# Optimization experiments

Measured on AMD Instinct MI355X. Metric: run time of the kernel, lower is better.

## Reference

```python
import jax, jax.numpy as jnp
import numpy as np

N_EMBD = 1024
N_HEAD = 16
LATENT = 64
HEAD_DIM = N_EMBD // N_HEAD
B, T = 2, 2048
SCALE = 1.0 / np.sqrt(LATENT)


def setup_inputs() -> dict:
    key = jax.random.key(0)
    ks = jax.random.split(key, 10)
    s = lambda fan_in: 1.0 / np.sqrt(fan_in)
    return {
        "x": jax.random.normal(ks[0], (B, T, N_EMBD), dtype=jnp.float32),
        "Wq": jax.random.normal(ks[1], (N_EMBD, N_EMBD), dtype=jnp.float32) * s(N_EMBD),
        "bq": jnp.zeros((N_EMBD,), dtype=jnp.float32),
        "Wk": jax.random.normal(ks[2], (N_EMBD, N_HEAD * LATENT), dtype=jnp.float32) * s(N_EMBD),
        "bk": jnp.zeros((N_HEAD * LATENT,), dtype=jnp.float32),
        "Wv": jax.random.normal(ks[3], (N_EMBD, N_HEAD * LATENT), dtype=jnp.float32) * s(N_EMBD),
        "bv": jnp.zeros((N_HEAD * LATENT,), dtype=jnp.float32),
        "Wo": jax.random.normal(ks[4], (N_HEAD * LATENT, N_EMBD), dtype=jnp.float32) * s(N_HEAD * LATENT),
        "bo": jnp.zeros((N_EMBD,), dtype=jnp.float32),
        "Wc": jax.random.normal(ks[5], (HEAD_DIM, LATENT), dtype=jnp.float32) * s(HEAD_DIM),
    }


def reference(x, Wq, bq, Wk, bk, Wv, bv, Wo, bo, Wc):
    Bv, Tv, C = x.shape
    # projections
    q = (x @ Wq + bq).reshape(Bv, Tv, N_HEAD, HEAD_DIM)        # [B,T,H,Dh]
    k = (x @ Wk + bk).reshape(Bv, Tv, N_HEAD, LATENT)          # [B,T,H,L]
    v = (x @ Wv + bv).reshape(Bv, Tv, N_HEAD, LATENT)          # [B,T,H,L]
    # compress q into latent dim: [B,T,H,L]
    qc = jnp.einsum("bthd,dl->bthl", q, Wc)
    # attention scores [B,H,T,T]
    att = jnp.einsum("bthl,bshl->bhts", qc, k) * SCALE
    causal = jnp.tril(jnp.ones((Tv, Tv), dtype=bool))
    att = jnp.where(causal[None, None], att, -jnp.inf)
    att = jax.nn.softmax(att, axis=-1)
    y = jnp.einsum("bhts,bshl->bthl", att, v).reshape(Bv, Tv, N_HEAD * LATENT)
    return y @ Wo + bo
```

## Files before the change

kernel.cpp:

```cpp
#include <hip/hip_runtime.h>
#include <stdint.h>

#define TT 2048
#define BB 2
#define MROWS (BB*TT)
#define LSCALE 0.18033688011112043f

typedef unsigned short u16;
typedef __bf16 bf16x8 __attribute__((ext_vector_type(8)));
typedef float f32x4 __attribute__((ext_vector_type(4)));
typedef short s16x8 __attribute__((ext_vector_type(8)));
typedef unsigned short u16x4 __attribute__((ext_vector_type(4)));

#define GLOBAL_AS const __attribute__((address_space(1))) void*
#define LDS_AS __attribute__((address_space(3))) void*

__device__ __forceinline__ u16 f2b(float f){
  uint32_t u = __builtin_bit_cast(uint32_t, f);
  u = (u + 0x7FFFu + ((u >> 16) & 1u)) >> 16;
  return (u16)u;
}

__global__ __launch_bounds__(256) void prep(
    const float* __restrict__ x, const float* __restrict__ Wq,
    const float* __restrict__ Wc, const float* __restrict__ bq,
    const float* __restrict__ Wk, const float* __restrict__ Wv,
    const float* __restrict__ Wo,
    u16* __restrict__ xb, u16* __restrict__ WqcT, u16* __restrict__ WkT,
    u16* __restrict__ WvT, u16* __restrict__ WoT, float* __restrict__ bqc){
  const int i = blockIdx.x, t = threadIdx.x;
  if (i < 4096){
    int id = i * 256 + t;
    float4 v = ((const float4*)x)[id];
    u16x4 o; o.x = f2b(v.x); o.y = f2b(v.y); o.z = f2b(v.z); o.w = f2b(v.w);
    ((u16x4*)xb)[id] = o;
    return;
  }
  if (i < 7168){
    int j = i - 4096;
    int z = j >> 10, rem = j & 1023;
    const float* in = (z == 0) ? Wk : (z == 1) ? Wv : Wo;
    u16* out = (z == 0) ? WkT : (z == 1) ? WvT : WoT;
    __shared__ float tl[32][33];
    int tx = t & 31, ty = t >> 5;
    int c0 = (rem & 31) * 32, r0 = (rem >> 5) * 32;
    #pragma unroll
    for (int k = 0; k < 32; k += 8)
      tl[ty + k][tx] = in[(size_t)(r0 + ty + k) * 1024 + c0 + tx];
    __syncthreads();
    #pragma unroll
    for (int k = 0; k < 32; k += 8)
      out[(size_t)(c0 + ty + k) * 1024 + r0 + tx] = f2b(tl[tx][ty + k]);
    return;
  }
  __shared__ float wc[4096];
  #pragma unroll
  for (int k = 0; k < 16; ++k) wc[k * 256 + t] = Wc[k * 256 + t];
  __syncthreads();
  if (i == 7424){
    #pragma unroll
    for (int k = 0; k < 4; ++k){
      int nn = t * 4 + k;
      int h = nn >> 6, lc = nn & 63;
      float a = 0.f;
      #pragma unroll
      for (int dd = 0; dd < 64; ++dd) a += bq[h * 64 + dd] * wc[dd * 64 + lc];
      bqc[nn] = a;
    }
    return;
  }
  __shared__ float tile[64][65];
  const int j = i - 7168;
  const int db = j >> 4, hb = j & 15;
  {
    int dl = t >> 2, lq = t & 3;
    const float4* wq4 = (const float4*)(Wq + (size_t)(db * 64 + dl) * 1024 + hb * 64);
    float wqr[64];
    #pragma unroll
    for (int k = 0; k < 16; ++k){
      float4 v = wq4[k];
      wqr[k * 4] = v.x; wqr[k * 4 + 1] = v.y; wqr[k * 4 + 2] = v.z; wqr[k * 4 + 3] = v.w;
    }
    #pragma unroll
    for (int jj = 0; jj < 16; ++jj){
      int lc = lq * 16 + jj;
      float a = 0.f;
      #pragma unroll
      for (int dd = 0; dd < 64; ++dd) a += wqr[dd] * wc[dd * 64 + lc];
      tile[dl][lc] = a;
    }
  }
  __syncthreads();
  {
    int nl = t >> 2, dq = t & 3;
    u16* dst = WqcT + (size_t)(hb * 64 + nl) * 1024 + db * 64 + dq * 16;
    #pragma unroll
    for (int k = 0; k < 16; ++k)
      dst[k] = f2b(tile[dq * 16 + k][nl]);
  }
}

__global__ void transpose_v(const u16* __restrict__ vb, u16* __restrict__ vt){
  __shared__ u16 t[32][34];
  int tx = threadIdx.x & 31, ty = threadIdx.x >> 5;
  int s0 = blockIdx.x * 32, d0 = blockIdx.y * 32, bh = blockIdx.z;
  int b = bh >> 4, h = bh & 15;
  #pragma unroll
  for (int i = 0; i < 32; i += 8)
    t[ty + i][tx] = vb[(size_t)(b * TT + s0 + ty + i) * 1024 + h * 64 + d0 + tx];
  __syncthreads();
  #pragma unroll
  for (int i = 0; i < 32; i += 8)
    vt[((size_t)bh * 64 + d0 + ty + i) * TT + s0 + tx] = t[tx][ty + i];
}

__device__ __forceinline__ void gemm_tile(const u16* __restrict__ A, const u16* __restrict__ BT,
                                          int m0, int n0, int K, f32x4 (&acc)[4][4],
                                          u16* As, u16* Bs, int tid){
  const int wv = tid >> 6, l = tid & 63;
  const int aoff = ((wv >> 1) * 64 + (l & 15)) * 32 + ((l >> 4) << 3);
  const int boff = ((wv & 1) * 64 + (l & 15)) * 32 + ((l >> 4) << 3);
  const int ob0 = wv * 1024 + l * 16;
  for (int kt = 0; kt < K; kt += 32){
    __syncthreads();
    #pragma unroll
    for (int j = 0; j < 2; ++j){
      int ob = ob0 + j * 4096;
      int row = ob >> 6, col = (ob & 63) >> 1;
      __builtin_amdgcn_global_load_lds((GLOBAL_AS)(A + (size_t)(m0 + row) * 1024 + kt + col),
                                       (LDS_AS)(As + wv * 512 + j * 2048), 16, 0, 0);
      __builtin_amdgcn_global_load_lds((GLOBAL_AS)(BT + (size_t)(n0 + row) * 1024 + kt + col),
                                       (LDS_AS)(Bs + wv * 512 + j * 2048), 16, 0, 0);
    }
    __syncthreads();
    bf16x8 av[4], bw[4];
    #pragma unroll
    for (int m = 0; m < 4; ++m) av[m] = *(const bf16x8*)(As + aoff + m * 512);
    #pragma unroll
    for (int n = 0; n < 4; ++n) bw[n] = *(const bf16x8*)(Bs + boff + n * 512);
    #pragma unroll
    for (int m = 0; m < 4; ++m)
      #pragma unroll
      for (int n = 0; n < 4; ++n)
        acc[m][n] = __builtin_amdgcn_mfma_f32_16x16x32_bf16(av[m], bw[n], acc[m][n], 0, 0, 0);
  }
}

__global__ __launch_bounds__(256) void gemm_qkv(
    const u16* __restrict__ xb,
    const u16* __restrict__ W0T, const u16* __restrict__ W1T, const u16* __restrict__ W2T,
    const float* __restrict__ b0, const float* __restrict__ b1, const float* __restrict__ b2,
    u16* __restrict__ o0, u16* __restrict__ o1, u16* __restrict__ o2){
  __shared__ u16 As[4096], Bs[4096];
  const int z = blockIdx.z;
  const u16* BT = (z == 0) ? W0T : (z == 1) ? W1T : W2T;
  const float* bias = (z == 0) ? b0 : (z == 1) ? b1 : b2;
  u16* Out = (z == 0) ? o0 : (z == 1) ? o1 : o2;
  const float osc = (z == 0) ? LSCALE : 1.0f;
  const int n0 = blockIdx.x * 128, m0 = blockIdx.y * 128;
  const int tid = threadIdx.x, wv = tid >> 6, l = tid & 63;
  f32x4 acc[4][4] = {};
  gemm_tile(xb, BT, m0, n0, 1024, acc, As, Bs, tid);
  const int wr = wv >> 1, wc = wv & 1;
  #pragma unroll
  for (int n = 0; n < 4; ++n){
    int col = n0 + wc * 64 + n * 16 + (l & 15);
    float bb = bias[col];
    #pragma unroll
    for (int m = 0; m < 4; ++m){
      int r0 = m0 + wr * 64 + m * 16 + ((l >> 4) << 2);
      #pragma unroll
      for (int r = 0; r < 4; ++r)
        Out[(size_t)(r0 + r) * 1024 + col] = f2b((acc[m][n][r] + bb) * osc);
    }
  }
}

__global__ __launch_bounds__(256) void gemm_o(
    const u16* __restrict__ A, const u16* __restrict__ BT,
    const float* __restrict__ bias, float* __restrict__ Out){
  __shared__ u16 As[2048], Bs[4096];
  const int n0 = blockIdx.x * 128, m0 = blockIdx.y * 64;
  const int tid = threadIdx.x, wv = tid >> 6, l = tid & 63;
  const int wr = wv >> 1, wc = wv & 1;
  const int aoff = (wr * 32 + (l & 15)) * 32 + ((l >> 4) << 3);
  const int boff = (wc * 64 + (l & 15)) * 32 + ((l >> 4) << 3);
  const int obA = wv * 1024 + l * 16;
  const int rowA = obA >> 6, colA = (obA & 63) >> 1;
  const int ob0 = wv * 1024 + l * 16;
  f32x4 acc[2][4] = {};
  for (int kt = 0; kt < 1024; kt += 32){
    __syncthreads();
    __builtin_amdgcn_global_load_lds((GLOBAL_AS)(A + (size_t)(m0 + rowA) * 1024 + kt + colA),
                                     (LDS_AS)(As + wv * 512), 16, 0, 0);
    #pragma unroll
    for (int j = 0; j < 2; ++j){
      int ob = ob0 + j * 4096;
      int row = ob >> 6, col = (ob & 63) >> 1;
      __builtin_amdgcn_global_load_lds((GLOBAL_AS)(BT + (size_t)(n0 + row) * 1024 + kt + col),
                                       (LDS_AS)(Bs + wv * 512 + j * 2048), 16, 0, 0);
    }
    __syncthreads();
    bf16x8 av[2], bw[4];
    #pragma unroll
    for (int m = 0; m < 2; ++m) av[m] = *(const bf16x8*)(As + aoff + m * 512);
    #pragma unroll
    for (int n = 0; n < 4; ++n) bw[n] = *(const bf16x8*)(Bs + boff + n * 512);
    #pragma unroll
    for (int m = 0; m < 2; ++m)
      #pragma unroll
      for (int n = 0; n < 4; ++n)
        acc[m][n] = __builtin_amdgcn_mfma_f32_16x16x32_bf16(av[m], bw[n], acc[m][n], 0, 0, 0);
  }
  #pragma unroll
  for (int n = 0; n < 4; ++n){
    int col = n0 + wc * 64 + n * 16 + (l & 15);
    float bb = bias[col];
    #pragma unroll
    for (int m = 0; m < 2; ++m){
      int r0 = m0 + wr * 32 + m * 16 + ((l >> 4) << 2);
      #pragma unroll
      for (int r = 0; r < 4; ++r)
        Out[(size_t)(r0 + r) * 1024 + col] = acc[m][n][r] + bb;
    }
  }
}

__global__ __launch_bounds__(256) void attn(
    const u16* __restrict__ qcg, const u16* __restrict__ kg,
    const u16* __restrict__ vtg, u16* __restrict__ yg){
  __shared__ u16 Ks[4096], Vs[4096];
  __shared__ u16 Ps[4096];
  const int idx = blockIdx.x;
  const int qt = 31 - (idx >> 5), bh = idx & 31;
  const int b = bh >> 4, h = bh & 15;
  const int q0 = qt * 64;
  const int tid = threadIdx.x, wv = tid >> 6, l = tid & 63;
  const int c4 = l >> 4, q16 = l & 15;
  const size_t base = (size_t)b * TT * 1024 + h * 64;
  const u16* Q = qcg + base;
  const u16* K = kg + base;
  const u16* Vt = vtg + (size_t)bh * 64 * TT;

  const int sr = tid >> 3;
  const int sc = (tid & 7) ^ (sr & 7);
  const u16* gK = K + (size_t)sr * 1024 + sc * 8;
  const u16* gV = Vt + (size_t)sr * TT + sc * 8;

  bf16x8 qf[2];
  {
    int qr = q0 + wv * 16 + q16;
    #pragma unroll
    for (int ks = 0; ks < 2; ++ks)
      qf[ks] = *(const bf16x8*)(Q + (size_t)qr * 1024 + ks * 32 + (c4 << 3));
  }
  f32x4 yacc[4] = {};
  float mrow = -1e30f, srow = 0.f;

  uint32_t* const PsW = (uint32_t*)Ps + wv * 512 + q16 * 32;
  const int pm = (q16 & 7) << 2;

  u16* const kd = Ks + wv * 512;
  u16* const vd = Vs + wv * 512;

  const int nt = qt + 1;
  for (int st = 0; st < nt; ++st){
    {
      const size_t o = (size_t)st * 64;
      __builtin_amdgcn_global_load_lds((GLOBAL_AS)(gK + o * 1024), (LDS_AS)kd, 16, 0, 0);
      __builtin_amdgcn_global_load_lds((GLOBAL_AS)(gK + (o + 32) * 1024), (LDS_AS)(kd + 2048), 16, 0, 0);
      __builtin_amdgcn_global_load_lds((GLOBAL_AS)(gV + o), (LDS_AS)vd, 16, 0, 0);
      __builtin_amdgcn_global_load_lds((GLOBAL_AS)(gV + o + 32 * TT), (LDS_AS)(vd + 2048), 16, 0, 0);
    }
    asm volatile("s_waitcnt vmcnt(0)" ::: "memory");
    __builtin_amdgcn_sched_barrier(0);
    __builtin_amdgcn_s_barrier();
    __builtin_amdgcn_sched_barrier(0);
    const int s0 = st * 64;
    f32x4 sf[4] = {};
    __builtin_amdgcn_s_setprio(1);
    #pragma unroll
    for (int ks = 0; ks < 2; ++ks)
      #pragma unroll
      for (int nf = 0; nf < 4; ++nf){
        int r = nf * 16 + q16, c = ks * 4 + c4;
        bf16x8 kf = *(const bf16x8*)(Ks + (r * 8 + (c ^ (r & 7))) * 8);
        sf[nf] = __builtin_amdgcn_mfma_f32_16x16x32_bf16(kf, qf[ks], sf[nf], 0, 0, 0);
      }
    __builtin_amdgcn_s_setprio(0);
    const int qa = q0 + wv * 16 + q16;
    float p[4][4];
    const bool domask = (st == qt);
    #pragma unroll
    for (int nf = 0; nf < 4; ++nf)
      #pragma unroll
      for (int r = 0; r < 4; ++r){
        float v_ = sf[nf][r];
        if (domask && (s0 + nf * 16 + c4 * 4 + r > qa)) v_ = -1e30f;
        p[nf][r] = v_;
      }
    float tmax = p[0][0];
    #pragma unroll
    for (int nf = 0; nf < 4; ++nf)
      #pragma unroll
      for (int r = 0; r < 4; ++r) tmax = fmaxf(tmax, p[nf][r]);
    tmax = fmaxf(tmax, __shfl_xor(tmax, 16));
    tmax = fmaxf(tmax, __shfl_xor(tmax, 32));
    if (__any(tmax > mrow + 8.0f)){
      float mnew = fmaxf(mrow, tmax);
      float resc = exp2f(mrow - mnew);
      srow *= resc;
      mrow = mnew;
      #pragma unroll
      for (int df = 0; df < 4; ++df)
        #pragma unroll
        for (int r = 0; r < 4; ++r) yacc[df][r] *= resc;
    }
    float tsum = 0.f;
    #pragma unroll
    for (int nf = 0; nf < 4; ++nf)
      #pragma unroll
      for (int r = 0; r < 4; ++r){ float e = exp2f(p[nf][r] - mrow); p[nf][r] = e; tsum += e; }
    tsum += __shfl_xor(tsum, 16);
    tsum += __shfl_xor(tsum, 32);
    srow += tsum;
    #pragma unroll
    for (int nf = 0; nf < 4; ++nf){
      uint32_t w0, w1;
      asm volatile("v_cvt_pk_bf16_f32 %0, %1, %2" : "=v"(w0) : "v"(p[nf][0]), "v"(p[nf][1]));
      asm volatile("v_cvt_pk_bf16_f32 %0, %1, %2" : "=v"(w1) : "v"(p[nf][2]), "v"(p[nf][3]));
      *(uint64_t*)(PsW + ((nf * 8 + c4 * 2) ^ pm)) = (uint64_t)w0 | ((uint64_t)w1 << 32);
    }
    asm volatile("s_waitcnt lgkmcnt(0)" ::: "memory");
    __builtin_amdgcn_sched_barrier(0);
    __builtin_amdgcn_s_setprio(1);
    #pragma unroll
    for (int ks2 = 0; ks2 < 2; ++ks2){
      bf16x8 pf = *(const bf16x8*)(PsW + ((ks2 * 16 + c4 * 4) ^ pm));
      #pragma unroll
      for (int df = 0; df < 4; ++df){
        int rd = df * 16 + q16, cd = ks2 * 4 + c4;
        bf16x8 vf = *(const bf16x8*)(Vs + (rd * 8 + (cd ^ (rd & 7))) * 8);
        yacc[df] = __builtin_amdgcn_mfma_f32_16x16x32_bf16(vf, pf, yacc[df], 0, 0, 0);
      }
    }
    __builtin_amdgcn_s_setprio(0);
    __builtin_amdgcn_s_barrier();
  }

  const float inv = 1.f / srow;
  const int qq = q0 + wv * 16 + q16;
  #pragma unroll
  for (int df = 0; df < 4; ++df){
    int d0 = df * 16 + c4 * 4;
    #pragma unroll
    for (int r = 0; r < 4; ++r)
      yg[(size_t)(b * TT + qq) * 1024 + h * 64 + d0 + r] = f2b(yacc[df][r] * inv);
  }
}

extern "C" void kernel_launch(void* const* d_in, const int* in_sizes, int n_in,
                              void* d_out, int out_size, void* d_ws, size_t ws_size,
                              hipStream_t stream){
  (void)in_sizes; (void)n_in; (void)out_size; (void)ws_size;
  const float* x  = (const float*)d_in[0];
  const float* Wq = (const float*)d_in[1];
  const float* bq = (const float*)d_in[2];
  const float* Wk = (const float*)d_in[3];
  const float* bk = (const float*)d_in[4];
  const float* Wv = (const float*)d_in[5];
  const float* bv = (const float*)d_in[6];
  const float* Wo = (const float*)d_in[7];
  const float* bo = (const float*)d_in[8];
  const float* Wc = (const float*)d_in[9];
  float* out = (float*)d_out;

  char* wsb = (char*)d_ws;
  u16* xb    = (u16*)(wsb);
  u16* yb    = (u16*)(wsb);
  u16* qcb   = (u16*)(wsb + (8u  << 20));
  u16* kb    = (u16*)(wsb + (16u << 20));
  u16* vb    = (u16*)(wsb + (24u << 20));
  u16* vtb   = (u16*)(wsb + (33u << 20));
  u16* WqcT  = (u16*)(wsb + (42u << 20));
  u16* WkT   = (u16*)(wsb + (44u << 20));
  u16* WvT   = (u16*)(wsb + (46u << 20));
  u16* WoT   = (u16*)(wsb + (48u << 20));
  float* bqc  = (float*)(wsb + (50u << 20));

  prep<<<7425, 256, 0, stream>>>(x, Wq, Wc, bq, Wk, Wv, Wo,
                                 xb, WqcT, WkT, WvT, WoT, bqc);
  gemm_qkv<<<dim3(8, 32, 3), 256, 0, stream>>>(xb, WqcT, WkT, WvT, bqc, bk, bv, qcb, kb, vb);
  transpose_v<<<dim3(64, 2, 32), 256, 0, stream>>>(vb, vtb);
  attn<<<dim3(1024), 256, 0, stream>>>(qcb, kb, vtb, yb);
  gemm_o<<<dim3(8, 64), 256, 0, stream>>>(yb, WoT, bo, out);
}
```

Measured before the change: 125.0 us.

## Compute softmax row sums via MFMA with ones and rebalance tile order

Result: faster. 122.2 us, median of 3 (-2.3%).

```diff
diff --git a/kernel.cpp b/kernel.cpp
--- a/kernel.cpp
+++ b/kernel.cpp
@@ -226,13 +226,20 @@
   }
 }
 
+__device__ const uint8_t qtab[32] = {
+  31, 30, 29, 28, 27, 26, 25, 24,
+   0,  1,  2,  3,  4,  5,  6,  7,
+  23, 22, 21, 20, 19, 18, 17, 16,
+   8,  9, 10, 11, 12, 13, 14, 15
+};
+
 __global__ __launch_bounds__(256) void attn(
     const u16* __restrict__ qcg, const u16* __restrict__ kg,
     const u16* __restrict__ vtg, u16* __restrict__ yg){
   __shared__ u16 Ks[4096], Vs[4096];
   __shared__ u16 Ps[4096];
   const int idx = blockIdx.x;
-  const int qt = 31 - (idx >> 5), bh = idx & 31;
+  const int qt = qtab[idx >> 5], bh = idx & 31;
   const int b = bh >> 4, h = bh & 15;
   const int q0 = qt * 64;
   const int tid = threadIdx.x, wv = tid >> 6, l = tid & 63;
@@ -254,8 +261,16 @@
     for (int ks = 0; ks < 2; ++ks)
       qf[ks] = *(const bf16x8*)(Q + (size_t)qr * 1024 + ks * 32 + (c4 << 3));
   }
+  bf16x8 ones;
+  {
+    s16x8 o1;
+    #pragma unroll
+    for (int j = 0; j < 8; ++j) o1[j] = (short)0x3F80;
+    ones = __builtin_bit_cast(bf16x8, o1);
+  }
   f32x4 yacc[4] = {};
-  float mrow = -1e30f, srow = 0.f;
+  f32x4 sacc = {};
+  float mrow = -1e30f;
 
   uint32_t* const PsW = (uint32_t*)Ps + wv * 512 + q16 * 32;
   const int pm = (q16 & 7) << 2;
@@ -299,31 +314,30 @@
         if (domask && (s0 + nf * 16 + c4 * 4 + r > qa)) v_ = -1e30f;
         p[nf][r] = v_;
       }
-    float tmax = p[0][0];
-    #pragma unroll
-    for (int nf = 0; nf < 4; ++nf)
-      #pragma unroll
-      for (int r = 0; r < 4; ++r) tmax = fmaxf(tmax, p[nf][r]);
+    float tmax = fmaxf(fmaxf(p[0][0], p[0][1]), p[0][2]);
+    tmax = fmaxf(fmaxf(tmax, p[0][3]), p[1][0]);
+    tmax = fmaxf(fmaxf(tmax, p[1][1]), p[1][2]);
+    tmax = fmaxf(fmaxf(tmax, p[1][3]), p[2][0]);
+    tmax = fmaxf(fmaxf(tmax, p[2][1]), p[2][2]);
+    tmax = fmaxf(fmaxf(tmax, p[2][3]), p[3][0]);
+    tmax = fmaxf(fmaxf(tmax, p[3][1]), p[3][2]);
+    tmax = fmaxf(tmax, p[3][3]);
     tmax = fmaxf(tmax, __shfl_xor(tmax, 16));
     tmax = fmaxf(tmax, __shfl_xor(tmax, 32));
     if (__any(tmax > mrow + 8.0f)){
       float mnew = fmaxf(mrow, tmax);
       float resc = exp2f(mrow - mnew);
-      srow *= resc;
+      sacc[0] *= resc;
       mrow = mnew;
       #pragma unroll
       for (int df = 0; df < 4; ++df)
         #pragma unroll
         for (int r = 0; r < 4; ++r) yacc[df][r] *= resc;
     }
-    float tsum = 0.f;
     #pragma unroll
     for (int nf = 0; nf < 4; ++nf)
       #pragma unroll
-      for (int r = 0; r < 4; ++r){ float e = exp2f(p[nf][r] - mrow); p[nf][r] = e; tsum += e; }
-    tsum += __shfl_xor(tsum, 16);
-    tsum += __shfl_xor(tsum, 32);
-    srow += tsum;
+      for (int r = 0; r < 4; ++r) p[nf][r] = exp2f(p[nf][r] - mrow);
     #pragma unroll
     for (int nf = 0; nf < 4; ++nf){
       uint32_t w0, w1;
@@ -337,6 +351,7 @@
     #pragma unroll
     for (int ks2 = 0; ks2 < 2; ++ks2){
       bf16x8 pf = *(const bf16x8*)(PsW + ((ks2 * 16 + c4 * 4) ^ pm));
+      sacc = __builtin_amdgcn_mfma_f32_16x16x32_bf16(ones, pf, sacc, 0, 0, 0);
       #pragma unroll
       for (int df = 0; df < 4; ++df){
         int rd = df * 16 + q16, cd = ks2 * 4 + c4;
@@ -348,7 +363,7 @@
     __builtin_amdgcn_s_barrier();
   }
 
-  const float inv = 1.f / srow;
+  const float inv = 1.f / sacc[0];
   const int qq = q0 + wv * 16 + q16;
   #pragma unroll
   for (int df = 0; df < 4; ++df){
```
